# Kernel tuning notes

Measured on AMD Instinct MI355X. Metric: run time of the kernel, lower is better.

Reference implementation:

```python
import jax, jax.numpy as jnp
import numpy as np


def setup_inputs() -> dict:
    key = jax.random.key(0)
    hidden_states = jax.random.normal(key, (8, 4096, 768), dtype=jnp.float32)
    return {"hidden_states": hidden_states}


def reference(hidden_states) -> jnp.ndarray:
    # fft along seq dim (-2), then along hidden dim (-1), keep real part.
    # Equivalent to a 2D FFT over the last two axes.
    x = hidden_states.astype(jnp.float32)
    out = jnp.fft.fft(jnp.fft.fft(x, axis=-2), axis=-1).real
    return out.astype(hidden_states.dtype)
```

## Files before the change

### kernel.cpp

```cpp
#include <hip/hip_runtime.h>
#include <hip/hip_bf16.h>

#define N1 4096
#define N2 768
#define NCC 384
#define CG 64
#define WS_NEEDED 100663296ull

__device__ __forceinline__ float2 cadd(float2 a, float2 b){ return make_float2(a.x+b.x, a.y+b.y); }
__device__ __forceinline__ float2 csub(float2 a, float2 b){ return make_float2(a.x-b.x, a.y-b.y); }
__device__ __forceinline__ float2 cmul(float2 a, float2 b){ return make_float2(a.x*b.x - a.y*b.y, a.x*b.y + a.y*b.x); }
__device__ __forceinline__ float2 cnegi(float2 a){ return make_float2(a.y, -a.x); }

__device__ __forceinline__ int rev6(int p) {
  int k = 0;
  #pragma unroll
  for (int i = 0; i < 6; ++i) { k = (k << 2) | (p & 3); p >>= 2; }
  return k;
}

__device__ __forceinline__ void fft8(float2 z[8]) {
  const float RH = 0.70710678118654752f;
  float2 u0=cadd(z[0],z[4]), v0=csub(z[0],z[4]);
  float2 u1=cadd(z[1],z[5]), v1=csub(z[1],z[5]);
  float2 u2=cadd(z[2],z[6]), v2=csub(z[2],z[6]);
  float2 u3=cadd(z[3],z[7]), v3=csub(z[3],z[7]);
  v1 = make_float2(RH*(v1.x+v1.y), RH*(v1.y-v1.x));
  v2 = cnegi(v2);
  v3 = make_float2(RH*(v3.y-v3.x), -RH*(v3.x+v3.y));
  float2 a0=cadd(u0,u2), b0=csub(u0,u2);
  float2 a1=cadd(u1,u3), b1=cnegi(csub(u1,u3));
  float2 c0=cadd(v0,v2), d0=csub(v0,v2);
  float2 c1=cadd(v1,v3), d1=cnegi(csub(v1,v3));
  z[0]=cadd(a0,a1); z[4]=csub(a0,a1);
  z[2]=cadd(b0,b1); z[6]=csub(b0,b1);
  z[1]=cadd(c0,c1); z[5]=csub(c0,c1);
  z[3]=cadd(d0,d1); z[7]=csub(d0,d1);
}

__global__ __launch_bounds__(512) void p1a_kernel(const float* __restrict__ x,
                                                  float2* __restrict__ ws) {
  __shared__ float2 T[4096];
  int bid = blockIdx.x;
  int b8  = bid & 7;
  int rem = bid >> 3;
  int cg  = rem / 64, a = rem % 64;
  const int t = threadIdx.x, l = t & 63, wv = t >> 6;

  const float* src = x + (size_t)b8 * N1 * N2 + 2*(cg*CG + l);
  float2 z[8];
  #pragma unroll
  for (int b1 = 0; b1 < 8; ++b1) {
    int row = a + 64*(8*b1 + wv);
    z[b1] = *reinterpret_cast<const float2*>(src + (size_t)row * N2);
  }
  fft8(z);
  float fac = -6.283185307179586f/64.0f * (float)wv;
  #pragma unroll
  for (int k0 = 1; k0 < 8; ++k0) {
    float sn, cs; __sincosf(fac * (float)k0, &sn, &cs);
    z[k0] = cmul(z[k0], make_float2(cs, sn));
  }
  #pragma unroll
  for (int k0 = 0; k0 < 8; ++k0) T[(k0*8 + wv)*64 + l] = z[k0];
  __syncthreads();
  #pragma unroll
  for (int b0 = 0; b0 < 8; ++b0) z[b0] = T[(wv*8 + b0)*64 + l];
  fft8(z);
  float fa = -6.283185307179586f/4096.0f * (float)a;
  #pragma unroll
  for (int k1 = 0; k1 < 8; ++k1) {
    int kb = 8*k1 + wv;
    float sn, cs; __sincosf(fa * (float)kb, &sn, &cs);
    float2 v = cmul(z[k1], make_float2(cs, sn));
    ws[(((size_t)b8*64 + kb)*64 + a)*NCC + cg*CG + l] = v;
  }
}

__global__ __launch_bounds__(1024) void p1b_kernel(const float2* __restrict__ ws,
                                                   float* __restrict__ out) {
  __shared__ float2 T[2][4096];
  int bid = blockIdx.x;
  int b8  = bid & 7;
  int rem = bid >> 3;
  int cg  = rem / 32, kbt = rem % 32;
  int kb0 = (kbt == 0) ? 0  : kbt;
  int kb1 = (kbt == 0) ? 32 : 64 - kbt;
  const int t = threadIdx.x, l = t & 63, wv = (t >> 6) & 7, ti = t >> 9;
  const int kb = ti ? kb1 : kb0;

  const float2* wsrc = ws + (((size_t)b8*64 + kb)*64)*NCC + cg*CG + l;
  float2 z[8];
  #pragma unroll
  for (int a1 = 0; a1 < 8; ++a1)
    z[a1] = wsrc[(size_t)(8*a1 + wv) * NCC];
  fft8(z);
  float fac = -6.283185307179586f/64.0f * (float)wv;
  #pragma unroll
  for (int q = 1; q < 8; ++q) {
    float sn, cs; __sincosf(fac * (float)q, &sn, &cs);
    z[q] = cmul(z[q], make_float2(cs, sn));
  }
  #pragma unroll
  for (int q = 0; q < 8; ++q) T[ti][(q*8 + wv)*64 + l] = z[q];
  __syncthreads();
  #pragma unroll
  for (int a0 = 0; a0 < 8; ++a0) z[a0] = T[ti][(wv*8 + a0)*64 + l];
  fft8(z);
  __syncthreads();
  #pragma unroll
  for (int ka1 = 0; ka1 < 8; ++ka1) T[ti][(8*ka1 + wv)*64 + l] = z[ka1];
  __syncthreads();

  const size_t obase = (size_t)b8 * N1 * N2;
  #pragma unroll
  for (int it = 0; it < 8; ++it) {
    int ka = 8*it + wv;
    int tj, kap;
    if (kbt == 0) { tj = ti; kap = ti ? (63 - ka) : ((64 - ka) & 63); }
    else          { tj = 1 - ti; kap = 63 - ka; }
    float2 Zk = T[ti][ka*64 + l];
    float2 Zp = T[tj][kap*64 + l];
    int r = kb + 64*ka;
    float2 o;
    if (r <= 2048) o = make_float2(0.5f*(Zk.x + Zp.x), 0.5f*(Zk.y + Zp.y));
    else           o = make_float2(0.5f*(Zp.y - Zk.y), 0.5f*(Zk.x - Zp.x));
    *reinterpret_cast<float2*>(out + obase + (size_t)r * N2 + 2*(cg*CG + l)) = o;
  }
}

#define PADI(i) ((i) + ((i) >> 4))
#define CPBUF 4352

__device__ __forceinline__ void bfly4p(float2* arr, int base, int M, float fac, int np) {
  float2 a0 = arr[PADI(base)], a1 = arr[PADI(base+M)];
  float2 a2 = arr[PADI(base+2*M)], a3 = arr[PADI(base+3*M)];
  float2 t0 = cadd(a0,a2), t1 = csub(a0,a2);
  float2 t2 = cadd(a1,a3), t3 = cnegi(csub(a1,a3));
  float2 y0 = cadd(t0,t2), y1 = cadd(t1,t3), y2 = csub(t0,t2), y3 = csub(t1,t3);
  float ang = fac * (float)np;
  float sn, cs; __sincosf(ang, &sn, &cs);
  float2 w1 = make_float2(cs, sn);
  float2 w2 = cmul(w1,w1);
  float2 w3 = cmul(w2,w1);
  arr[PADI(base)]     = y0;
  arr[PADI(base+M)]   = cmul(y1,w1);
  arr[PADI(base+2*M)] = cmul(y2,w2);
  arr[PADI(base+3*M)] = cmul(y3,w3);
}

__global__ __launch_bounds__(1024) void fft_seq_fused(const float* __restrict__ x,
                                                      float* __restrict__ out) {
  extern __shared__ float2 lds[];
  int bid = blockIdx.x;
  int wg  = (bid & 7) * 96 + (bid >> 3);
  int b   = wg / 96;
  int g   = wg % 96;
  const int t = threadIdx.x;
  const size_t base = (size_t)b * N1 * N2 + 8 * (size_t)g;

  for (int r = t; r < N1; r += 1024) {
    const float* p = x + base + (size_t)r * N2;
    float4 A  = *reinterpret_cast<const float4*>(p);
    float4 Bv = *reinterpret_cast<const float4*>(p + 4);
    int ip = PADI(r);
    lds[ip]             = make_float2(A.x, A.y);
    lds[CPBUF + ip]     = make_float2(A.z, A.w);
    lds[2*CPBUF + ip]   = make_float2(Bv.x, Bv.y);
    lds[3*CPBUF + ip]   = make_float2(Bv.z, Bv.w);
  }
  __syncthreads();

  const int wv  = t >> 6;
  const int cp  = wv & 3;
  const int idx = ((wv >> 2) << 6) + (t & 63);
  float2* buf = lds + cp * CPBUF;

  #pragma unroll
  for (int s = 0; s < 6; ++s) {
    int lm = 10 - 2*s;
    int M  = 1 << lm;
    float fac = -6.283185307179586f / (float)(4*M);
    #pragma unroll
    for (int jj = 0; jj < 4; ++jj) {
      int j   = idx + (jj << 8);
      int np  = j & (M-1);
      int grp = j >> lm;
      int bse = (grp << (lm+2)) + np;
      bfly4p(buf, bse, M, fac, np);
    }
    __syncthreads();
  }

  float* orow = out + base;
  #pragma unroll
  for (int i = 0; i < 4; ++i) {
    int k  = ((t & 63) << 6) + (t >> 6) + (i << 4);
    int km = (N1 - k) & (N1 - 1);
    int pk = PADI(rev6(k));
    int pn = PADI(rev6(km));
    float o[8];
    #pragma unroll
    for (int c = 0; c < 4; ++c) {
      float2 zk = lds[c*CPBUF + pk];
      float2 zn = lds[c*CPBUF + pn];
      if (k <= 2048) { o[2*c] = 0.5f*(zk.x + zn.x); o[2*c+1] = 0.5f*(zk.y + zn.y); }
      else           { o[2*c] = 0.5f*(zn.y - zk.y); o[2*c+1] = 0.5f*(zk.x - zn.x); }
    }
    float* q = orow + (size_t)k * N2;
    *reinterpret_cast<float4*>(q)     = make_float4(o[0], o[1], o[2], o[3]);
    *reinterpret_cast<float4*>(q + 4) = make_float4(o[4], o[5], o[6], o[7]);
  }
}

__global__ __launch_bounds__(256) void fft_hid_kernel(float* __restrict__ out) {
  __shared__ float T[4][12*69];
  const int grp = threadIdx.x >> 6;
  const int l   = threadIdx.x & 63;
  int task = blockIdx.x * 4 + grp;
  int b  = task / 2049;
  int t1 = task - b * 2049;
  const bool special = (t1 == 0) || (t1 == 2048);
  float* baseB = out + (size_t)b * N1 * N2;
  float* pre = baseB + (size_t)t1 * N2;
  float* pim = baseB + (size_t)(N1 - t1) * N2;

  float2 z[12];
  #pragma unroll
  for (int m = 0; m < 12; ++m) {
    float re = pre[(m << 6) + l];
    float im = special ? 0.0f : pim[(m << 6) + l];
    z[m] = make_float2(re, im);
  }

  float2 A[3][4];
  #pragma unroll
  for (int q = 0; q < 3; ++q) {
    float2 s0 = z[q], s1 = z[3+q], s2 = z[6+q], s3 = z[9+q];
    float2 t0 = cadd(s0,s2), t1v = csub(s0,s2);
    float2 t2 = cadd(s1,s3), t3 = cnegi(csub(s1,s3));
    A[q][0] = cadd(t0,t2); A[q][1] = cadd(t1v,t3);
    A[q][2] = csub(t0,t2); A[q][3] = csub(t1v,t3);
  }
  const float h3 = 0.8660254037844386f;
  const float2 W1[4] = { {1.f,0.f}, {h3,-0.5f}, {0.5f,-h3}, {0.f,-1.f} };
  const float2 W2[4] = { {1.f,0.f}, {0.5f,-h3}, {-0.5f,-h3}, {-1.f,0.f} };
  float2 y[12];
  #pragma unroll
  for (int k4 = 0; k4 < 4; ++k4) {
    float2 C0 = A[0][k4];
    float2 C1 = cmul(A[1][k4], W1[k4]);
    float2 C2 = cmul(A[2][k4], W2[k4]);
    float2 tt = cadd(C1,C2), d = csub(C1,C2);
    float2 u  = make_float2(C0.x - 0.5f*tt.x, C0.y - 0.5f*tt.y);
    float2 idd = make_float2(h3*d.y, -h3*d.x);
    y[k4]   = cadd(C0, tt);
    y[k4+4] = cadd(u, idd);
    y[k4+8] = csub(u, idd);
  }

  float base = -6.283185307179586f * (float)l / 768.0f;
  #pragma unroll
  for (int km = 1; km < 12; ++km) {
    float sn, cs; __sincosf(base * (float)km, &sn, &cs);
    y[km] = cmul(y[km], make_float2(cs, sn));
  }

  #pragma unroll
  for (int st = 0; st < 6; ++st) {
    int h = 32 >> st;
    int j = l & (h - 1);
    float sn, cs; __sincosf(-3.14159265358979f * (float)j / (float)h, &sn, &cs);
    float2 w = make_float2(cs, sn);
    bool hi = (l & h) != 0;
    #pragma unroll
    for (int m = 0; m < 12; ++m) {
      float px = __shfl_xor(y[m].x, h, 64);
      float py = __shfl_xor(y[m].y, h, 64);
      float2 p = make_float2(px, py);
      float2 lo  = cadd(y[m], p);
      float2 hiv = cmul(csub(p, y[m]), w);
      y[m] = hi ? hiv : lo;
    }
  }

  int r = ((l&1)<<5)|((l&2)<<3)|((l&4)<<1)|((l&8)>>1)|((l&16)>>3)|((l&32)>>5);
  float* Tb = T[grp];
  #pragma unroll
  for (int km = 0; km < 12; ++km) Tb[km*69 + r] = y[km].x;
  __syncthreads();

  #pragma unroll
  for (int mp = 0; mp < 12; ++mp) {
    int k = (mp << 6) + l;
    float v = Tb[(k % 12)*69 + (k / 12)];
    pre[k] = v;
    if (!special) pim[(N2 - k) % N2] = v;
  }
}

extern "C" void kernel_launch(void* const* d_in, const int* in_sizes, int n_in,
                              void* d_out, int out_size, void* d_ws, size_t ws_size,
                              hipStream_t stream) {
  const float* x = (const float*)d_in[0];
  float* out = (float*)d_out;
  if (ws_size >= WS_NEEDED) {
    float2* ws = (float2*)d_ws;
    p1a_kernel<<<dim3(3072), dim3(512), 0, stream>>>(x, ws);
    p1b_kernel<<<dim3(1536), dim3(1024), 0, stream>>>(ws, out);
  } else {
    (void)hipFuncSetAttribute(reinterpret_cast<const void*>(&fft_seq_fused),
                              hipFuncAttributeMaxDynamicSharedMemorySize,
                              4 * CPBUF * (int)sizeof(float2));
    fft_seq_fused<<<dim3(768), dim3(1024), 4 * CPBUF * sizeof(float2), stream>>>(x, out);
  }
  fft_hid_kernel<<<dim3(4098), dim3(256), 0, stream>>>(out);
}
```

Measured before the change: 108.7 us.

## Widen p1a tiles to 128 columns with float4 coalesced loads via LDS staging

```diff
diff --git a/kernel.cpp b/kernel.cpp
--- a/kernel.cpp
+++ b/kernel.cpp
@@ -38,42 +38,56 @@
   z[3]=cadd(d0,d1); z[7]=csub(d0,d1);
 }
 
-__global__ __launch_bounds__(512) void p1a_kernel(const float* __restrict__ x,
-                                                  float2* __restrict__ ws) {
-  __shared__ float2 T[4096];
+__global__ __launch_bounds__(1024) void p1a_kernel(const float* __restrict__ x,
+                                                   float2* __restrict__ ws) {
+  __shared__ float4 S4[64*65];
+  float2* S = reinterpret_cast<float2*>(S4);
   int bid = blockIdx.x;
   int b8  = bid & 7;
   int rem = bid >> 3;
-  int cg  = rem / 64, a = rem % 64;
-  const int t = threadIdx.x, l = t & 63, wv = t >> 6;
-
-  const float* src = x + (size_t)b8 * N1 * N2 + 2*(cg*CG + l);
+  int cg  = rem / 64;
+  int a   = rem % 64;
+  const int t = threadIdx.x, l = t & 63, w = t >> 6;
+
+  const float* src = x + (size_t)b8 * N1 * N2 + (size_t)cg * 256;
+  #pragma unroll
+  for (int j = 0; j < 4; ++j) {
+    int r   = 4*w + j;
+    int row = a + 64*r;
+    float4 v = *reinterpret_cast<const float4*>(src + (size_t)row * N2 + 4*l);
+    S4[r*65 + l] = v;
+  }
+  __syncthreads();
+
+  const int c = t & 127, b0 = t >> 7;
   float2 z[8];
   #pragma unroll
-  for (int b1 = 0; b1 < 8; ++b1) {
-    int row = a + 64*(8*b1 + wv);
-    z[b1] = *reinterpret_cast<const float2*>(src + (size_t)row * N2);
-  }
+  for (int b1 = 0; b1 < 8; ++b1) z[b1] = S[(8*b1 + b0)*130 + c];
   fft8(z);
-  float fac = -6.283185307179586f/64.0f * (float)wv;
-  #pragma unroll
-  for (int k0 = 1; k0 < 8; ++k0) {
-    float sn, cs; __sincosf(fac * (float)k0, &sn, &cs);
-    z[k0] = cmul(z[k0], make_float2(cs, sn));
-  }
-  #pragma unroll
-  for (int k0 = 0; k0 < 8; ++k0) T[(k0*8 + wv)*64 + l] = z[k0];
-  __syncthreads();
-  #pragma unroll
-  for (int b0 = 0; b0 < 8; ++b0) z[b0] = T[(wv*8 + b0)*64 + l];
+  {
+    float sn, cs; __sincosf(-6.283185307179586f/64.f * (float)b0, &sn, &cs);
+    float2 wstep = make_float2(cs, sn), wcur = wstep;
+    #pragma unroll
+    for (int j = 1; j < 8; ++j) { z[j] = cmul(z[j], wcur); wcur = cmul(wcur, wstep); }
+  }
+  __syncthreads();
+  #pragma unroll
+  for (int j = 0; j < 8; ++j) S[(j*8 + b0)*130 + c] = z[j];
+  __syncthreads();
+
+  const int jj = t >> 7;
+  #pragma unroll
+  for (int b0i = 0; b0i < 8; ++b0i) z[b0i] = S[(jj*8 + b0i)*130 + c];
   fft8(z);
-  float fa = -6.283185307179586f/4096.0f * (float)a;
-  #pragma unroll
-  for (int k1 = 0; k1 < 8; ++k1) {
-    int kb = 8*k1 + wv;
-    float sn, cs; __sincosf(fa * (float)kb, &sn, &cs);
-    float2 v = cmul(z[k1], make_float2(cs, sn));
-    ws[(((size_t)b8*64 + kb)*64 + a)*NCC + cg*CG + l] = v;
+  float2 wc, w8;
+  { float sn, cs; __sincosf(-6.283185307179586f/4096.f * (float)(a*jj), &sn, &cs); wc = make_float2(cs, sn); }
+  { float sn, cs; __sincosf(-6.283185307179586f/4096.f * (float)(8*a),  &sn, &cs); w8 = make_float2(cs, sn); }
+  float2* wdst = ws + ((size_t)b8*64)*64*NCC + (size_t)a*NCC + cg*128 + c;
+  #pragma unroll
+  for (int m = 0; m < 8; ++m) {
+    int kb = 8*m + jj;
+    wdst[(size_t)kb * 64 * NCC] = cmul(z[m], wc);
+    wc = cmul(wc, w8);
   }
 }
 
@@ -306,7 +320,7 @@
   float* out = (float*)d_out;
   if (ws_size >= WS_NEEDED) {
     float2* ws = (float2*)d_ws;
-    p1a_kernel<<<dim3(3072), dim3(512), 0, stream>>>(x, ws);
+    p1a_kernel<<<dim3(1536), dim3(1024), 0, stream>>>(x, ws);
     p1b_kernel<<<dim3(1536), dim3(1024), 0, stream>>>(ws, out);
   } else {
     (void)hipFuncSetAttribute(reinterpret_cast<const void*>(&fft_seq_fused),
```

Result: slower. 111.0 us (+2.0%).
